# Performance work log

Hardware: AMD Instinct MI355X
Metric: run time of the kernel (lower is better)

The kernel has to match this reference:

```python
import jax, jax.numpy as jnp
import numpy as np

TAU = 1.0


def setup_inputs() -> dict:
    key = jax.random.key(0)
    k1, k2 = jax.random.split(key)
    B, D, F = 32, 2048, 512
    x = jax.random.normal(k1, (B, D, F), dtype=jnp.float32)
    # keras random_uniform(0, 0.001) initializer
    sorting_vector = jax.random.uniform(k2, (D,), dtype=jnp.float32) * 0.001
    return {"x": x, "sorting_vector": sorting_vector}


def reference(x, sorting_vector):
    # NeuralSort-style permutation matrix.
    # A_s[i,j] = |s[j] - s[i]|; B[i,j] = sum_k |s[j] - s[k]| (row-constant in i)
    s = sorting_vector  # [D]
    D = s.shape[0]
    abs_sum = jnp.sum(jnp.abs(s[None, :] - s[:, None]), axis=0)  # [D]
    # multiplication_factor[i] = D + 1 - 2*(i+1)
    scal = (D + 1.0 - 2.0 * (jnp.arange(D, dtype=s.dtype) + 1.0))  # [D]
    logits = (scal[:, None] * s[None, :] - abs_sum[None, :]) / TAU  # [D, D]
    P = jax.nn.softmax(logits, axis=-1)  # [D, D]
    # tensordot(x, P, [[1],[0]]) -> [B, F, D], then transpose back to [B, D, F]
    out = jnp.einsum('bdf,dj->bjf', x, P)
    return out
```

## Files before the change

kernel.cpp:

```cpp
#include <hip/hip_runtime.h>
#include <cstdint>

#define Bsz 32
#define Dd 2048
#define Ff 512
#define TT 16
#define NC 32
#define DC (Dd / NC)


__global__ __launch_bounds__(256) void k_prep(const float* __restrict__ s,
                                              float* __restrict__ abs_sum,
                                              float* __restrict__ q) {
  __shared__ float sk[256];
  int t = threadIdx.x;
  int j = blockIdx.x * 256 + t;
  float sj = s[j];
  float acc = 0.f;
  for (int c = 0; c < Dd; c += 256) {
    __syncthreads();
    sk[t] = s[c + t];
    __syncthreads();
#pragma unroll 16
    for (int k = 0; k < 256; k += 4) {
      float4 sv = *(const float4*)&sk[k];
      acc += fabsf(sj - sv.x) + fabsf(sj - sv.y) + fabsf(sj - sv.z) + fabsf(sj - sv.w);
    }
  }
  abs_sum[j] = acc;
  float v = 2048.0f * sj;
  float p = __expf(-acc);
  float4 q0, q1, q2, q3;
  q0.x = p;
  p *= v;                q0.y = p;
  p *= v * 0.5f;         q0.z = p;
  p *= v * (1.f / 3.f);  q0.w = p;
  p *= v * 0.25f;        q1.x = p;
  p *= v * 0.2f;         q1.y = p;
  p *= v * (1.f / 6.f);  q1.z = p;
  p *= v * (1.f / 7.f);  q1.w = p;
  p *= v * 0.125f;       q2.x = p;
  p *= v * (1.f / 9.f);  q2.y = p;
  p *= v * 0.1f;         q2.z = p;
  p *= v * (1.f / 11.f); q2.w = p;
  p *= v * (1.f / 12.f); q3.x = p;
  p *= v * (1.f / 13.f); q3.y = p;
  p *= v * (1.f / 14.f); q3.z = p;
  p *= v * (1.f / 15.f); q3.w = p;
  float4* qv = (float4*)&q[(size_t)j * TT];
  qv[0] = q0; qv[1] = q1; qv[2] = q2; qv[3] = q3;
}

__global__ __launch_bounds__(256) void k_wd(const float* __restrict__ s,
                                            const float* __restrict__ abs_sum,
                                            float* __restrict__ coeff) {
  int w = threadIdx.x >> 6, l = threadIdx.x & 63;
  int d = blockIdx.x * 4 + w;
  float scal = 2047.0f - 2.0f * (float)d;
  float sum = 0.f;
#pragma unroll
  for (int it = 0; it < 32; ++it) {
    int j = it * 64 + l;
    sum += __expf(fmaf(scal, s[j], -abs_sum[j]));
  }
#pragma unroll
  for (int off = 32; off > 0; off >>= 1) sum += __shfl_xor(sum, off, 64);
  float wd = 1.0f / sum;
  float u = scal * (1.0f / 2048.0f);
  if (l < TT) {
    float p = wd;
    for (int k = 0; k < l; ++k) p *= u;
    coeff[(size_t)d * TT + l] = p;
  }
}

__global__ __launch_bounds__(256) void k_mom(const float* __restrict__ x,
                                             const float* __restrict__ coeff,
                                             float* __restrict__ Yp) {
  __shared__ float cf[DC * TT];
  int t = threadIdx.x;
  int b = blockIdx.x;
  int ch = blockIdx.y;
  *(float4*)&cf[t * 4] = *(const float4*)&coeff[(size_t)ch * DC * TT + t * 4];
  __syncthreads();

  const float* xb = x + ((size_t)b * Dd + (size_t)ch * DC) * Ff + 2 * t;
  float2 acc[TT];
#pragma unroll
  for (int tt = 0; tt < TT; ++tt) acc[tt] = make_float2(0.f, 0.f);

#pragma unroll 4
  for (int d = 0; d < DC; ++d) {
    float2 xv = *(const float2*)&xb[(size_t)d * Ff];
    const float4* cp = (const float4*)&cf[d * TT];
    float cfr[TT];
    *(float4*)&cfr[0] = cp[0];
    *(float4*)&cfr[4] = cp[1];
    *(float4*)&cfr[8] = cp[2];
    *(float4*)&cfr[12] = cp[3];
#pragma unroll
    for (int tt = 0; tt < TT; ++tt) {
      acc[tt].x = fmaf(cfr[tt], xv.x, acc[tt].x);
      acc[tt].y = fmaf(cfr[tt], xv.y, acc[tt].y);
    }
  }

  float* yp = Yp + ((size_t)(ch * Bsz + b) * TT) * Ff + 2 * t;
#pragma unroll
  for (int tt = 0; tt < TT; ++tt)
    *(float2*)&yp[(size_t)tt * Ff] = acc[tt];
}

__global__ __launch_bounds__(256) void k_red(const float* __restrict__ Yp,
                                             float* __restrict__ Y) {
  int i = (blockIdx.x * 256 + threadIdx.x) * 4;
  float4 a = make_float4(0.f, 0.f, 0.f, 0.f);
#pragma unroll 8
  for (int c = 0; c < NC; ++c) {
    float4 v = *(const float4*)&Yp[(size_t)c * (Bsz * TT * Ff) + i];
    a.x += v.x; a.y += v.y; a.z += v.z; a.w += v.w;
  }
  *(float4*)&Y[i] = a;
}

__global__ __launch_bounds__(256) void k_out(const float* __restrict__ Y,
                                             const float* __restrict__ q,
                                             float* __restrict__ out) {
  __shared__ float qs[64 * TT];
  int t = threadIdx.x;
  int b = blockIdx.x;
  int j0 = blockIdx.y * 64;
  *(float4*)&qs[t * 4] = *(const float4*)&q[(size_t)j0 * TT + t * 4];
  __syncthreads();

  const float* yb = Y + (size_t)b * TT * Ff + 2 * t;
  float2 y[TT];
#pragma unroll
  for (int tt = 0; tt < TT; ++tt) y[tt] = *(const float2*)&yb[(size_t)tt * Ff];

  float* ob = out + ((size_t)b * Dd + j0) * Ff + 2 * t;
  for (int j = 0; j < 64; ++j) {
    const float4* qp = (const float4*)&qs[j * TT];
    float qr[TT];
    *(float4*)&qr[0] = qp[0];
    *(float4*)&qr[4] = qp[1];
    *(float4*)&qr[8] = qp[2];
    *(float4*)&qr[12] = qp[3];
    float ox0 = 0.f, ox1 = 0.f, oy0 = 0.f, oy1 = 0.f;
#pragma unroll
    for (int tt = 0; tt < TT; tt += 2) {
      ox0 = fmaf(qr[tt], y[tt].x, ox0);
      oy0 = fmaf(qr[tt], y[tt].y, oy0);
      ox1 = fmaf(qr[tt + 1], y[tt + 1].x, ox1);
      oy1 = fmaf(qr[tt + 1], y[tt + 1].y, oy1);
    }
    *(float2*)&ob[(size_t)j * Ff] = make_float2(ox0 + ox1, oy0 + oy1);
  }
}

extern "C" void kernel_launch(void* const* d_in, const int* in_sizes, int n_in,
                              void* d_out, int out_size, void* d_ws, size_t ws_size,
                              hipStream_t stream) {
  const float* x = (const float*)d_in[0];
  const float* s = (const float*)d_in[1];
  float* out = (float*)d_out;

  char* ws = (char*)d_ws;
  float* abs_sum = (float*)ws;
  float* q = (float*)(ws + 8192);
  float* coeff = (float*)(ws + 8192 + 131072);
  float* Y = (float*)(ws + 8192 + 262144);
  float* Yp = (float*)(ws + 8192 + 262144 + 1048576);

  k_prep<<<Dd / 256, 256, 0, stream>>>(s, abs_sum, q);
  k_wd<<<Dd / 4, 256, 0, stream>>>(s, abs_sum, coeff);
  k_mom<<<dim3(Bsz, NC), 256, 0, stream>>>(x, coeff, Yp);
  k_red<<<(Bsz * TT * Ff) / (256 * 4), 256, 0, stream>>>(Yp, Y);
  k_out<<<dim3(Bsz, Dd / 64), 256, 0, stream>>>(Y, q, out);
}
```

Before: 286.6 us.

## Replace split-D moment kernel and global reduction with F-tiled in-block reduction

The moment pass over x is re-partitioned so each block owns a 64-column F tile over the full D range, with 8 thread groups splitting D and reducing through shared memory. This removes the partial-sum buffer Yp and the separate reduction kernel. The output kernel also switches to float4 stores with two j-groups per block. The moment kernel now launches 256 blocks instead of 1024, which may lower occupancy and latency hiding. Its x reads are also narrower, 256-byte row segments per group.

```diff
diff --git a/kernel.cpp b/kernel.cpp
--- a/kernel.cpp
+++ b/kernel.cpp
@@ -5,8 +5,8 @@
 #define Dd 2048
 #define Ff 512
 #define TT 16
-#define NC 32
-#define DC (Dd / NC)
+#define FT 64
+#define RG 8
 
 
 __global__ __launch_bounds__(256) void k_prep(const float* __restrict__ s,
@@ -74,53 +74,65 @@
   }
 }
 
-__global__ __launch_bounds__(256) void k_mom(const float* __restrict__ x,
-                                             const float* __restrict__ coeff,
-                                             float* __restrict__ Yp) {
-  __shared__ float cf[DC * TT];
+__global__ __launch_bounds__(256) void k_y(const float* __restrict__ x,
+                                           const float* __restrict__ coeff,
+                                           float* __restrict__ Y) {
+  __shared__ float cf[256 * TT];
+  __shared__ float red[RG * TT * FT];
   int t = threadIdx.x;
   int b = blockIdx.x;
-  int ch = blockIdx.y;
-  *(float4*)&cf[t * 4] = *(const float4*)&coeff[(size_t)ch * DC * TT + t * 4];
-  __syncthreads();
+  int f0 = blockIdx.y * FT;
+  int g = t >> 5;
+  int fp = t & 31;
 
-  const float* xb = x + ((size_t)b * Dd + (size_t)ch * DC) * Ff + 2 * t;
+  const float* xb = x + (size_t)b * Dd * Ff + f0 + fp * 2;
   float2 acc[TT];
 #pragma unroll
   for (int tt = 0; tt < TT; ++tt) acc[tt] = make_float2(0.f, 0.f);
 
-#pragma unroll 4
-  for (int d = 0; d < DC; ++d) {
-    float2 xv = *(const float2*)&xb[(size_t)d * Ff];
-    const float4* cp = (const float4*)&cf[d * TT];
-    float cfr[TT];
-    *(float4*)&cfr[0] = cp[0];
-    *(float4*)&cfr[4] = cp[1];
-    *(float4*)&cfr[8] = cp[2];
-    *(float4*)&cfr[12] = cp[3];
+  for (int c = 0; c < Dd / 256; ++c) {
+    __syncthreads();
+    {
+      const float4* src = (const float4*)&coeff[(size_t)c * 256 * TT];
+      float4* dst = (float4*)cf;
 #pragma unroll
-    for (int tt = 0; tt < TT; ++tt) {
-      acc[tt].x = fmaf(cfr[tt], xv.x, acc[tt].x);
-      acc[tt].y = fmaf(cfr[tt], xv.y, acc[tt].y);
+      for (int r = 0; r < 4; ++r) dst[t + r * 256] = src[t + r * 256];
+    }
+    __syncthreads();
+#pragma unroll 8
+    for (int i = 0; i < 32; ++i) {
+      int lr = i * 8 + g;
+      float2 xv = *(const float2*)&xb[(size_t)(c * 256 + lr) * Ff];
+      const float4* cp = (const float4*)&cf[lr * TT];
+      float cfr[TT];
+      *(float4*)&cfr[0] = cp[0];
+      *(float4*)&cfr[4] = cp[1];
+      *(float4*)&cfr[8] = cp[2];
+      *(float4*)&cfr[12] = cp[3];
+#pragma unroll
+      for (int tt = 0; tt < TT; ++tt) {
+        acc[tt].x = fmaf(cfr[tt], xv.x, acc[tt].x);
+        acc[tt].y = fmaf(cfr[tt], xv.y, acc[tt].y);
+      }
     }
   }
 
-  float* yp = Yp + ((size_t)(ch * Bsz + b) * TT) * Ff + 2 * t;
+  __syncthreads();
 #pragma unroll
   for (int tt = 0; tt < TT; ++tt)
-    *(float2*)&yp[(size_t)tt * Ff] = acc[tt];
-}
+    *(float2*)&red[(g * TT + tt) * FT + fp * 2] = acc[tt];
+  __syncthreads();
 
-__global__ __launch_bounds__(256) void k_red(const float* __restrict__ Yp,
-                                             float* __restrict__ Y) {
-  int i = (blockIdx.x * 256 + threadIdx.x) * 4;
-  float4 a = make_float4(0.f, 0.f, 0.f, 0.f);
-#pragma unroll 8
-  for (int c = 0; c < NC; ++c) {
-    float4 v = *(const float4*)&Yp[(size_t)c * (Bsz * TT * Ff) + i];
-    a.x += v.x; a.y += v.y; a.z += v.z; a.w += v.w;
+  float* Yb = Y + (size_t)b * TT * Ff + f0;
+#pragma unroll
+  for (int r = 0; r < 4; ++r) {
+    int oi = t + r * 256;
+    int tt = oi >> 6, fl = oi & 63;
+    float sum = 0.f;
+#pragma unroll
+    for (int gg = 0; gg < RG; ++gg) sum += red[(gg * TT + tt) * FT + fl];
+    Yb[(size_t)tt * Ff + fl] = sum;
   }
-  *(float4*)&Y[i] = a;
 }
 
 __global__ __launch_bounds__(256) void k_out(const float* __restrict__ Y,
@@ -133,28 +145,37 @@
   *(float4*)&qs[t * 4] = *(const float4*)&q[(size_t)j0 * TT + t * 4];
   __syncthreads();
 
-  const float* yb = Y + (size_t)b * TT * Ff + 2 * t;
-  float2 y[TT];
+  int fi = t & 127;
+  int jg = t >> 7;
+
+  const float* yb = Y + (size_t)b * TT * Ff + fi * 4;
+  float4 y[TT];
 #pragma unroll
-  for (int tt = 0; tt < TT; ++tt) y[tt] = *(const float2*)&yb[(size_t)tt * Ff];
+  for (int tt = 0; tt < TT; ++tt) y[tt] = *(const float4*)&yb[(size_t)tt * Ff];
 
-  float* ob = out + ((size_t)b * Dd + j0) * Ff + 2 * t;
-  for (int j = 0; j < 64; ++j) {
-    const float4* qp = (const float4*)&qs[j * TT];
+  float* ob = out + ((size_t)b * Dd + j0 + jg * 32) * Ff + fi * 4;
+  for (int j = 0; j < 32; ++j) {
+    const float4* qp = (const float4*)&qs[(jg * 32 + j) * TT];
     float qr[TT];
     *(float4*)&qr[0] = qp[0];
     *(float4*)&qr[4] = qp[1];
     *(float4*)&qr[8] = qp[2];
     *(float4*)&qr[12] = qp[3];
-    float ox0 = 0.f, ox1 = 0.f, oy0 = 0.f, oy1 = 0.f;
+    float4 o0 = make_float4(0.f, 0.f, 0.f, 0.f);
+    float4 o1 = make_float4(0.f, 0.f, 0.f, 0.f);
 #pragma unroll
     for (int tt = 0; tt < TT; tt += 2) {
-      ox0 = fmaf(qr[tt], y[tt].x, ox0);
-      oy0 = fmaf(qr[tt], y[tt].y, oy0);
-      ox1 = fmaf(qr[tt + 1], y[tt + 1].x, ox1);
-      oy1 = fmaf(qr[tt + 1], y[tt + 1].y, oy1);
+      o0.x = fmaf(qr[tt], y[tt].x, o0.x);
+      o0.y = fmaf(qr[tt], y[tt].y, o0.y);
+      o0.z = fmaf(qr[tt], y[tt].z, o0.z);
+      o0.w = fmaf(qr[tt], y[tt].w, o0.w);
+      o1.x = fmaf(qr[tt + 1], y[tt + 1].x, o1.x);
+      o1.y = fmaf(qr[tt + 1], y[tt + 1].y, o1.y);
+      o1.z = fmaf(qr[tt + 1], y[tt + 1].z, o1.z);
+      o1.w = fmaf(qr[tt + 1], y[tt + 1].w, o1.w);
     }
-    *(float2*)&ob[(size_t)j * Ff] = make_float2(ox0 + ox1, oy0 + oy1);
+    float4 o = make_float4(o0.x + o1.x, o0.y + o1.y, o0.z + o1.z, o0.w + o1.w);
+    *(float4*)&ob[(size_t)j * Ff] = o;
   }
 }
 
@@ -170,11 +191,9 @@
   float* q = (float*)(ws + 8192);
   float* coeff = (float*)(ws + 8192 + 131072);
   float* Y = (float*)(ws + 8192 + 262144);
-  float* Yp = (float*)(ws + 8192 + 262144 + 1048576);
 
   k_prep<<<Dd / 256, 256, 0, stream>>>(s, abs_sum, q);
   k_wd<<<Dd / 4, 256, 0, stream>>>(s, abs_sum, coeff);
-  k_mom<<<dim3(Bsz, NC), 256, 0, stream>>>(x, coeff, Yp);
-  k_red<<<(Bsz * TT * Ff) / (256 * 4), 256, 0, stream>>>(Yp, Y);
+  k_y<<<dim3(Bsz, Ff / FT), 256, 0, stream>>>(x, coeff, Y);
   k_out<<<dim3(Bsz, Dd / 64), 256, 0, stream>>>(Y, q, out);
 }
```

Measured after the change: 386.7 us. 1.35x slower.
